# Kernel optimization log

Hardware: AMD Instinct MI355X
Metric: run time of the kernel (lower is better)

## Reference

```python
import jax, jax.numpy as jnp
import numpy as np
from jax import lax

WIN = 9
EPS = 1e-05


def _box_sum(v, win):
    # v: [B, 1, D, H, W]
    pad = win // 2
    dn = lax.conv_dimension_numbers(v.shape, (1, 1, win, win, win), ('NCDHW', 'OIDHW', 'NCDHW'))
    k = jnp.ones((win,), v.dtype)
    # apply 1D sum along D, H, W in turn
    v = lax.conv_general_dilated(v, k.reshape(1, 1, win, 1, 1), (1, 1, 1), [(pad, pad), (0, 0), (0, 0)], dimension_numbers=dn)
    v = lax.conv_general_dilated(v, k.reshape(1, 1, 1, win, 1), (1, 1, 1), [(0, 0), (pad, pad), (0, 0)], dimension_numbers=dn)
    v = lax.conv_general_dilated(v, k.reshape(1, 1, 1, 1, win), (1, 1, 1), [(0, 0), (0, 0), (pad, pad)], dimension_numbers=dn)
    return v


def setup_inputs() -> dict:
    key = jax.random.key(0)
    k1, k2 = jax.random.split(key)
    shape = (2, 1, 160, 192, 160)
    x = jax.random.uniform(k1, shape, dtype=jnp.float32)
    y = jax.random.uniform(k2, shape, dtype=jnp.float32)
    return {"x": x, "y": y}


def reference(x, y):
    win = WIN
    win_size = float(win ** 3)
    x_sum = _box_sum(x, win)
    y_sum = _box_sum(y, win)
    x2_sum = _box_sum(x * x, win)
    y2_sum = _box_sum(y * y, win)
    xy_sum = _box_sum(x * y, win)
    cross = xy_sum - x_sum * y_sum / win_size
    x_var = jnp.maximum(x2_sum - x_sum * x_sum / win_size, EPS)
    y_var = jnp.maximum(y2_sum - y_sum * y_sum / win_size, EPS)
    cc = cross * cross / (x_var * y_var)
    return -jnp.mean(cc)
```

## Files before the change

### kernel.cpp

```cpp
#include <hip/hip_runtime.h>

#define BB 2
#define DD 160
#define HH 192
#define WW 160
#define HW (HH * WW)
#define PAD 4
#define TH 16
#define TW 32
#define EXTH 24
#define EXTW 40
#define XSTR 40
#define APL 960
#define WRS 36
#define WCSTR 868
#define HRS 36
#define HCSTR 580
#define CHUNK 19
#define NCH 9
#define NITER 27
#define WT (WW / TW)
#define HT (HH / TH)
#define NBLK (WT * HT * NCH * BB)
#define NTASK 480
#define EPS 1e-5f
#define INV_WS (1.0f / 729.0f)

__device__ __forceinline__ void bar_lgkm() {
  asm volatile("s_waitcnt lgkmcnt(0)" ::: "memory");
  __builtin_amdgcn_s_barrier();
  asm volatile("" ::: "memory");
}

__device__ __forceinline__ float4 f4add(float4 a, float4 b) {
  return make_float4(a.x + b.x, a.y + b.y, a.z + b.z, a.w + b.w);
}
__device__ __forceinline__ float4 f4pm(float4 s, float4 p, float4 m) {
  return make_float4(s.x + p.x - m.x, s.y + p.y - m.y,
                     s.z + p.z - m.z, s.w + p.w - m.w);
}

__global__ void __launch_bounds__(256) k_lncc(
    const float* __restrict__ x, const float* __restrict__ y,
    float* __restrict__ partials)
{
  __shared__ __align__(16) float sb[2 * APL];
  __shared__ __align__(16) float ws[5 * WCSTR];
  __shared__ __align__(16) float hs[5 * HCSTR];
  __shared__ float red[4];

  const int t = threadIdx.x;
  const int w0 = blockIdx.x * TW;
  const int h0 = blockIdx.y * TH;
  const int bz = blockIdx.z;
  const int b = bz / NCH;
  const int chunk = bz - b * NCH;
  const int dc0 = chunk * CHUNK;
  const int g0 = dc0 - PAD;

  for (int i = t; i < 2 * APL; i += 256) sb[i] = 0.f;

  int la0, la1; bool tk0, tk1;
  const float* gp0; const float* gp1;
  {
    const float* bx = x + (long)b * DD * HW;
    const float* by = y + (long)b * DD * HW;
#define MKTASK(TAU, LA, TK, GP)                                           \
    {                                                                     \
      int tau = (TAU);                                                    \
      int a = tau / 240;                                                  \
      int rem = tau - 240 * a;                                            \
      int r = rem / 10;                                                   \
      int q = rem - 10 * r;                                               \
      int aa = (a < 2) ? a : 0;                                           \
      int gh = h0 - PAD + r;                                              \
      int gw = w0 - PAD + 4 * q;                                          \
      bool ok = (tau < NTASK) && ((unsigned)gh < (unsigned)HH) &&         \
                ((unsigned)gw < (unsigned)WW);                            \
      LA = aa * APL + r * XSTR + 4 * q;                                   \
      TK = ok;                                                            \
      GP = (aa ? by : bx) + (ok ? (gh * WW + gw) : 0);                    \
    }
    MKTASK(t, la0, tk0, gp0)
    MKTASK(t + 256, la1, tk1, gp1)
#undef MKTASK
  }

  const int r2 = t >> 3;
  const int qq = t & 7;
  const int rdx = r2 * XSTR + 4 * qq;
  const int wwr = r2 * WRS + 4 * qq;

  const int wq3 = t & 7;
  const int hf3 = (t >> 3) & 1;
  const int c3 = t >> 4;
  const int rb3 = c3 * WCSTR + (hf3 * 8) * WRS + 4 * wq3;
  const int wb3 = c3 * HCSTR + (hf3 * 8) * HRS + 4 * wq3;

  const int h4 = t >> 4, p4 = t & 15;
  const int hrOff = h4 * HRS + 2 * p4;

  float2 rg[9][5];
#pragma unroll
  for (int i = 0; i < 9; ++i)
#pragma unroll
    for (int c = 0; c < 5; ++c) { rg[i][c].x = 0.f; rg[i][c].y = 0.f; }
  float2 rn0 = {0, 0}, rn1 = {0, 0}, rn2 = {0, 0}, rn3 = {0, 0}, rn4 = {0, 0};
  float acc = 0.f;

  __syncthreads();

  float4 st0 = make_float4(0, 0, 0, 0), st1 = st0;
  bool ps0 = false, ps1 = false;
  if (g0 >= 0) {
    const long so = (long)g0 * HW;
    ps0 = tk0; if (ps0) st0 = *(const float4*)(gp0 + so);
    ps1 = tk1; if (ps1) st1 = *(const float4*)(gp1 + so);
  }

  for (int ko = 0; ko < 3; ++ko) {
#pragma unroll
    for (int jj = 0; jj < 9; ++jj) {
      const int k = ko * 9 + jj;
      const int g = g0 + k;
      const bool gv = ((unsigned)g < (unsigned)DD);

      if (gv) {
        if (ps0) *(float4*)&sb[la0] = st0;
        if (ps1) *(float4*)&sb[la1] = st1;
      }
      {
        const int gn = g + 1;
        const bool nv = (k + 1 < NITER) && ((unsigned)gn < (unsigned)DD);
        const long so = (long)gn * HW;
        ps0 = tk0 && nv; if (ps0) st0 = *(const float4*)(gp0 + so);
        ps1 = tk1 && nv; if (ps1) st1 = *(const float4*)(gp1 + so);
      }

      float2 hv0 = {0, 0}, hv1 = {0, 0}, hv2 = {0, 0}, hv3 = {0, 0}, hv4 = {0, 0};
      if (gv) {
        bar_lgkm();
        if (t < 192) {
          float xa[12], ya[12];
          {
            float4 X0 = *(const float4*)&sb[rdx];
            float4 X1 = *(const float4*)&sb[rdx + 4];
            float4 X2 = *(const float4*)&sb[rdx + 8];
            xa[0]=X0.x; xa[1]=X0.y; xa[2]=X0.z; xa[3]=X0.w;
            xa[4]=X1.x; xa[5]=X1.y; xa[6]=X1.z; xa[7]=X1.w;
            xa[8]=X2.x; xa[9]=X2.y; xa[10]=X2.z; xa[11]=X2.w;
            float4 Y0 = *(const float4*)&sb[APL + rdx];
            float4 Y1 = *(const float4*)&sb[APL + rdx + 4];
            float4 Y2 = *(const float4*)&sb[APL + rdx + 8];
            ya[0]=Y0.x; ya[1]=Y0.y; ya[2]=Y0.z; ya[3]=Y0.w;
            ya[4]=Y1.x; ya[5]=Y1.y; ya[6]=Y1.z; ya[7]=Y1.w;
            ya[8]=Y2.x; ya[9]=Y2.y; ya[10]=Y2.z; ya[11]=Y2.w;
          }
#define EMITCH(CIDX, EXPR)                                                 \
          {                                                                \
            float qv[12];                                                  \
            _Pragma("unroll")                                              \
            for (int i = 0; i < 12; ++i) qv[i] = (EXPR);                   \
            float o0 = ((qv[0]+qv[1])+(qv[2]+qv[3]))+                      \
                       ((qv[4]+qv[5])+(qv[6]+qv[7]))+qv[8];                \
            float o1 = o0 + qv[9]  - qv[0];                                \
            float o2 = o1 + qv[10] - qv[1];                                \
            float o3 = o2 + qv[11] - qv[2];                                \
            *(float4*)&ws[(CIDX) * WCSTR + wwr] = make_float4(o0,o1,o2,o3);\
          }
          EMITCH(0, xa[i])
          EMITCH(1, ya[i])
          EMITCH(2, xa[i] * xa[i])
          EMITCH(3, ya[i] * ya[i])
          EMITCH(4, xa[i] * ya[i])
#undef EMITCH
        }
        bar_lgkm();
        if (t < 80) {
          float4 v[16];
#pragma unroll
          for (int i = 0; i < 9; ++i) v[i] = *(const float4*)&ws[rb3 + i * WRS];
          float4 s = f4add(f4add(f4add(f4add(v[0], v[1]), f4add(v[2], v[3])),
                                 f4add(f4add(v[4], v[5]), f4add(v[6], v[7]))),
                           v[8]);
          *(float4*)&hs[wb3] = s;
#pragma unroll
          for (int hh = 1; hh < 8; ++hh) {
            v[hh + 8] = *(const float4*)&ws[rb3 + (hh + 8) * WRS];
            s = f4pm(s, v[hh + 8], v[hh - 1]);
            *(float4*)&hs[wb3 + hh * HRS] = s;
          }
        }
        bar_lgkm();
        hv0 = *(const float2*)&hs[hrOff];
        hv1 = *(const float2*)&hs[HCSTR + hrOff];
        hv2 = *(const float2*)&hs[2 * HCSTR + hrOff];
        hv3 = *(const float2*)&hs[3 * HCSTR + hrOff];
        hv4 = *(const float2*)&hs[4 * HCSTR + hrOff];
      }

      rn0.x += hv0.x - rg[jj][0].x; rg[jj][0].x = hv0.x;
      rn0.y += hv0.y - rg[jj][0].y; rg[jj][0].y = hv0.y;
      rn1.x += hv1.x - rg[jj][1].x; rg[jj][1].x = hv1.x;
      rn1.y += hv1.y - rg[jj][1].y; rg[jj][1].y = hv1.y;
      rn2.x += hv2.x - rg[jj][2].x; rg[jj][2].x = hv2.x;
      rn2.y += hv2.y - rg[jj][2].y; rg[jj][2].y = hv2.y;
      rn3.x += hv3.x - rg[jj][3].x; rg[jj][3].x = hv3.x;
      rn3.y += hv3.y - rg[jj][3].y; rg[jj][3].y = hv3.y;
      rn4.x += hv4.x - rg[jj][4].x; rg[jj][4].x = hv4.x;
      rn4.y += hv4.y - rg[jj][4].y; rg[jj][4].y = hv4.y;

      if (k >= 8) {
        const int d = dc0 + (k - 8);
        if (d < DD) {
          {
            float cross = fmaf(-rn0.x * INV_WS, rn1.x, rn4.x);
            float xv = fmaxf(fmaf(-rn0.x * INV_WS, rn0.x, rn2.x), EPS);
            float yv = fmaxf(fmaf(-rn1.x * INV_WS, rn1.x, rn3.x), EPS);
            acc += (cross * cross) * __builtin_amdgcn_rcpf(xv * yv);
          }
          {
            float cross = fmaf(-rn0.y * INV_WS, rn1.y, rn4.y);
            float xv = fmaxf(fmaf(-rn0.y * INV_WS, rn0.y, rn2.y), EPS);
            float yv = fmaxf(fmaf(-rn1.y * INV_WS, rn1.y, rn3.y), EPS);
            acc += (cross * cross) * __builtin_amdgcn_rcpf(xv * yv);
          }
        }
      }
    }
  }

#pragma unroll
  for (int o = 32; o > 0; o >>= 1) acc += __shfl_down(acc, o);
  if ((t & 63) == 0) red[t >> 6] = acc;
  __syncthreads();
  if (t == 0) {
    int bid = (bz * HT + blockIdx.y) * WT + blockIdx.x;
    partials[bid] = (red[0] + red[1]) + (red[2] + red[3]);
  }
}

__global__ void __launch_bounds__(256) k_finalize(
    const float* __restrict__ partials, float* __restrict__ out)
{
  __shared__ double red[256];
  double s = 0.0;
  for (int i = threadIdx.x; i < NBLK; i += 256) s += (double)partials[i];
  red[threadIdx.x] = s;
  __syncthreads();
  for (int o = 128; o > 0; o >>= 1) {
    if (threadIdx.x < o) red[threadIdx.x] += red[threadIdx.x + o];
    __syncthreads();
  }
  if (threadIdx.x == 0) {
    const double Nvox = (double)BB * DD * HH * WW;
    out[0] = (float)(-red[0] / Nvox);
  }
}

extern "C" void kernel_launch(void* const* d_in, const int* in_sizes, int n_in,
                              void* d_out, int out_size, void* d_ws, size_t ws_size,
                              hipStream_t stream) {
  (void)in_sizes; (void)n_in; (void)out_size; (void)ws_size;
  const float* x = (const float*)d_in[0];
  const float* y = (const float*)d_in[1];
  float* out = (float*)d_out;
  float* partials = (float*)d_ws;

  dim3 grid(WT, HT, BB * NCH);
  k_lncc<<<grid, 256, 0, stream>>>(x, y, partials);
  k_finalize<<<1, 256, 0, stream>>>(partials, out);
}
```

Before: 81.86 us.

## Restructure slice pipeline to two barriers with double-distance prefetch

Reorders each depth step so the W-pass reads the current slice from shared memory before the next slice is written. This cuts the per-iteration barriers from three to two, and global prefetch now runs two slices ahead. The H-pass is also reassigned from 80 threads doing 8 rows each to 40 threads doing all 16 rows, which lengthens the serial running-sum chain per thread. The first slice is preloaded into shared memory before the loop. Risks are less parallelism in the H-pass, more registers per thread, and the barriers now run even on invalid slices.

```diff
diff --git a/kernel.cpp b/kernel.cpp
--- a/kernel.cpp
+++ b/kernel.cpp
@@ -91,11 +91,9 @@
   const int rdx = r2 * XSTR + 4 * qq;
   const int wwr = r2 * WRS + 4 * qq;
 
-  const int wq3 = t & 7;
-  const int hf3 = (t >> 3) & 1;
-  const int c3 = t >> 4;
-  const int rb3 = c3 * WCSTR + (hf3 * 8) * WRS + 4 * wq3;
-  const int wb3 = c3 * HCSTR + (hf3 * 8) * HRS + 4 * wq3;
+  const int c3 = t / 8, wq3 = t - 8 * c3;
+  const int rb3 = c3 * WCSTR + 4 * wq3;
+  const int wb3 = c3 * HCSTR + 4 * wq3;
 
   const int h4 = t >> 4, p4 = t & 15;
   const int hrOff = h4 * HRS + 2 * p4;
@@ -112,11 +110,19 @@
 
   float4 st0 = make_float4(0, 0, 0, 0), st1 = st0;
   bool ps0 = false, ps1 = false;
-  if (g0 >= 0) {
-    const long so = (long)g0 * HW;
-    ps0 = tk0; if (ps0) st0 = *(const float4*)(gp0 + so);
-    ps1 = tk1; if (ps1) st1 = *(const float4*)(gp1 + so);
-  }
+  {
+    if ((unsigned)g0 < (unsigned)DD) {
+      const long so = (long)g0 * HW;
+      if (tk0) *(float4*)&sb[la0] = *(const float4*)(gp0 + so);
+      if (tk1) *(float4*)&sb[la1] = *(const float4*)(gp1 + so);
+    }
+    const int g1i = g0 + 1;
+    const bool v1 = ((unsigned)g1i < (unsigned)DD);
+    const long so1 = (long)g1i * HW;
+    ps0 = tk0 && v1; if (ps0) st0 = *(const float4*)(gp0 + so1);
+    ps1 = tk1 && v1; if (ps1) st1 = *(const float4*)(gp1 + so1);
+  }
+  __syncthreads();
 
   for (int ko = 0; ko < 3; ++ko) {
 #pragma unroll
@@ -125,73 +131,76 @@
       const int g = g0 + k;
       const bool gv = ((unsigned)g < (unsigned)DD);
 
-      if (gv) {
-        if (ps0) *(float4*)&sb[la0] = st0;
-        if (ps1) *(float4*)&sb[la1] = st1;
-      }
+      if (gv && t < 192) {
+        float xa[12], ya[12];
+        {
+          float4 X0 = *(const float4*)&sb[rdx];
+          float4 X1 = *(const float4*)&sb[rdx + 4];
+          float4 X2 = *(const float4*)&sb[rdx + 8];
+          xa[0]=X0.x; xa[1]=X0.y; xa[2]=X0.z; xa[3]=X0.w;
+          xa[4]=X1.x; xa[5]=X1.y; xa[6]=X1.z; xa[7]=X1.w;
+          xa[8]=X2.x; xa[9]=X2.y; xa[10]=X2.z; xa[11]=X2.w;
+          float4 Y0 = *(const float4*)&sb[APL + rdx];
+          float4 Y1 = *(const float4*)&sb[APL + rdx + 4];
+          float4 Y2 = *(const float4*)&sb[APL + rdx + 8];
+          ya[0]=Y0.x; ya[1]=Y0.y; ya[2]=Y0.z; ya[3]=Y0.w;
+          ya[4]=Y1.x; ya[5]=Y1.y; ya[6]=Y1.z; ya[7]=Y1.w;
+          ya[8]=Y2.x; ya[9]=Y2.y; ya[10]=Y2.z; ya[11]=Y2.w;
+        }
+#define EMITCH(CIDX, EXPR)                                                 \
+        {                                                                  \
+          float qv[12];                                                    \
+          _Pragma("unroll")                                                \
+          for (int i = 0; i < 12; ++i) qv[i] = (EXPR);                     \
+          float o0 = ((qv[0]+qv[1])+(qv[2]+qv[3]))+                        \
+                     ((qv[4]+qv[5])+(qv[6]+qv[7]))+qv[8];                  \
+          float o1 = o0 + qv[9]  - qv[0];                                  \
+          float o2 = o1 + qv[10] - qv[1];                                  \
+          float o3 = o2 + qv[11] - qv[2];                                  \
+          *(float4*)&ws[(CIDX) * WCSTR + wwr] = make_float4(o0,o1,o2,o3);  \
+        }
+        EMITCH(0, xa[i])
+        EMITCH(1, ya[i])
+        EMITCH(2, xa[i] * xa[i])
+        EMITCH(3, ya[i] * ya[i])
+        EMITCH(4, xa[i] * ya[i])
+#undef EMITCH
+      }
+
+      bar_lgkm();
+
+      if (ps0) *(float4*)&sb[la0] = st0;
+      if (ps1) *(float4*)&sb[la1] = st1;
+
       {
-        const int gn = g + 1;
-        const bool nv = (k + 1 < NITER) && ((unsigned)gn < (unsigned)DD);
+        const int gn = g + 2;
+        const bool nv = (k + 2 < NITER) && ((unsigned)gn < (unsigned)DD);
         const long so = (long)gn * HW;
         ps0 = tk0 && nv; if (ps0) st0 = *(const float4*)(gp0 + so);
         ps1 = tk1 && nv; if (ps1) st1 = *(const float4*)(gp1 + so);
       }
 
-      float2 hv0 = {0, 0}, hv1 = {0, 0}, hv2 = {0, 0}, hv3 = {0, 0}, hv4 = {0, 0};
+      if (gv && t < 40) {
+        float4 v[24];
+#pragma unroll
+        for (int i = 0; i < 9; ++i) v[i] = *(const float4*)&ws[rb3 + i * WRS];
+        float4 s = f4add(f4add(f4add(f4add(v[0], v[1]), f4add(v[2], v[3])),
+                               f4add(f4add(v[4], v[5]), f4add(v[6], v[7]))),
+                         v[8]);
+        *(float4*)&hs[wb3] = s;
+#pragma unroll
+        for (int hh = 1; hh < TH; ++hh) {
+          v[hh + 8] = *(const float4*)&ws[rb3 + (hh + 8) * WRS];
+          s = f4pm(s, v[hh + 8], v[hh - 1]);
+          *(float4*)&hs[wb3 + hh * HRS] = s;
+        }
+      }
+
+      bar_lgkm();
+
+      float2 hv0 = {0, 0}, hv1 = {0, 0}, hv2 = {0, 0},
+             hv3 = {0, 0}, hv4 = {0, 0};
       if (gv) {
-        bar_lgkm();
-        if (t < 192) {
-          float xa[12], ya[12];
-          {
-            float4 X0 = *(const float4*)&sb[rdx];
-            float4 X1 = *(const float4*)&sb[rdx + 4];
-            float4 X2 = *(const float4*)&sb[rdx + 8];
-            xa[0]=X0.x; xa[1]=X0.y; xa[2]=X0.z; xa[3]=X0.w;
-            xa[4]=X1.x; xa[5]=X1.y; xa[6]=X1.z; xa[7]=X1.w;
-            xa[8]=X2.x; xa[9]=X2.y; xa[10]=X2.z; xa[11]=X2.w;
-            float4 Y0 = *(const float4*)&sb[APL + rdx];
-            float4 Y1 = *(const float4*)&sb[APL + rdx + 4];
-            float4 Y2 = *(const float4*)&sb[APL + rdx + 8];
-            ya[0]=Y0.x; ya[1]=Y0.y; ya[2]=Y0.z; ya[3]=Y0.w;
-            ya[4]=Y1.x; ya[5]=Y1.y; ya[6]=Y1.z; ya[7]=Y1.w;
-            ya[8]=Y2.x; ya[9]=Y2.y; ya[10]=Y2.z; ya[11]=Y2.w;
-          }
-#define EMITCH(CIDX, EXPR)                                                 \
-          {                                                                \
-            float qv[12];                                                  \
-            _Pragma("unroll")                                              \
-            for (int i = 0; i < 12; ++i) qv[i] = (EXPR);                   \
-            float o0 = ((qv[0]+qv[1])+(qv[2]+qv[3]))+                      \
-                       ((qv[4]+qv[5])+(qv[6]+qv[7]))+qv[8];                \
-            float o1 = o0 + qv[9]  - qv[0];                                \
-            float o2 = o1 + qv[10] - qv[1];                                \
-            float o3 = o2 + qv[11] - qv[2];                                \
-            *(float4*)&ws[(CIDX) * WCSTR + wwr] = make_float4(o0,o1,o2,o3);\
-          }
-          EMITCH(0, xa[i])
-          EMITCH(1, ya[i])
-          EMITCH(2, xa[i] * xa[i])
-          EMITCH(3, ya[i] * ya[i])
-          EMITCH(4, xa[i] * ya[i])
-#undef EMITCH
-        }
-        bar_lgkm();
-        if (t < 80) {
-          float4 v[16];
-#pragma unroll
-          for (int i = 0; i < 9; ++i) v[i] = *(const float4*)&ws[rb3 + i * WRS];
-          float4 s = f4add(f4add(f4add(f4add(v[0], v[1]), f4add(v[2], v[3])),
-                                 f4add(f4add(v[4], v[5]), f4add(v[6], v[7]))),
-                           v[8]);
-          *(float4*)&hs[wb3] = s;
-#pragma unroll
-          for (int hh = 1; hh < 8; ++hh) {
-            v[hh + 8] = *(const float4*)&ws[rb3 + (hh + 8) * WRS];
-            s = f4pm(s, v[hh + 8], v[hh - 1]);
-            *(float4*)&hs[wb3 + hh * HRS] = s;
-          }
-        }
-        bar_lgkm();
         hv0 = *(const float2*)&hs[hrOff];
         hv1 = *(const float2*)&hs[HCSTR + hrOff];
         hv2 = *(const float2*)&hs[2 * HCSTR + hrOff];
```

Result: slower. 99.37 us (+21.4%).
